# Kernel tuning notes

Measured on AMD Instinct MI355X. Metric: run time of the kernel, lower is better.

Reference implementation:

```python
import jax, jax.numpy as jnp
import numpy as np

N, E, F_IN, H, HEADS, L = 50000, 800000, 64, 64, 4, 5
NEG_SLOPE = 0.2  # PyG GATv2 default negative_slope


def _gatv2(h, src, dst, Wl, bl, Wr, br, att, bias, n):
    # PyG GATv2Conv, concat=False: x_l = lin_l(x), x_r = lin_r(x)
    xl = (h @ Wl + bl).reshape(n, HEADS, H)
    xr = (h @ Wr + br).reshape(n, HEADS, H)
    # per-edge score: a^T LeakyReLU(x_l[src] + x_r[dst])  -> [E', heads]
    z = jax.nn.leaky_relu(xl[src] + xr[dst], NEG_SLOPE)
    e = jnp.einsum('ehc,hc->eh', z, att)
    # segment softmax over incoming edges of each dst node
    m = jax.lax.stop_gradient(jax.ops.segment_max(e, dst, num_segments=n))
    ex = jnp.exp(e - m[dst])
    s = jax.ops.segment_sum(ex, dst, num_segments=n)
    alpha = ex / s[dst]
    out = jax.ops.segment_sum(xl[src] * alpha[:, :, None], dst, num_segments=n)
    return out.mean(axis=1) + bias  # concat=False -> mean over heads, + bias


def _forward(node_features, Wl, bl, Wr, br, att, gat_bias,
             Wm1, bm1, Wm2, bm2, Wp, bp, Wv1, bv1, Wv2, bv2,
             src, dst, current_pos, valid_neighbors, owned_nodes):
    n = node_features.shape[0]
    h = node_features
    for i in range(L):  # depth = 5 since N > 15
        h_new = jax.nn.elu(_gatv2(h, src, dst, Wl[i], bl[i], Wr[i], br[i], att[i], gat_bias[i], n))
        h = h_new if i == 0 else h + h_new  # residual after first layer
    cand = jnp.concatenate([jnp.asarray([current_pos], dtype=valid_neighbors.dtype), valid_neighbors])
    curr = h[current_pos]
    pairs = jnp.concatenate([jnp.broadcast_to(curr, (cand.shape[0], curr.shape[0])), h[cand]], axis=1)
    move_logits = (jax.nn.relu(pairs @ Wm1 + bm1) @ Wm2 + bm2)[:, 0]
    price_logits = h[owned_nodes] @ Wp + bp
    g = jnp.concatenate([h.mean(axis=0), curr])
    value = (jax.nn.relu(g @ Wv1 + bv1) @ Wv2 + bv2)[0]
    return move_logits, price_logits, value


def setup_inputs() -> dict:
    key = jax.random.key(0)
    ks = jax.random.split(key, 24)
    s = 0.05
    return {
        'node_features': jax.random.normal(ks[0], (N, F_IN), jnp.float32),
        'edge_index': jax.random.randint(ks[1], (2, E), 0, N),
        'current_pos': 7,
        'valid_neighbors': jax.random.randint(ks[2], (8,), 0, N),
        'owned_nodes': jax.random.randint(ks[3], (10,), 0, N),
        'Wl': jax.random.normal(ks[4], (L, F_IN, HEADS * H), jnp.float32) * s,
        'bl': jnp.zeros((L, HEADS * H), jnp.float32),
        'Wr': jax.random.normal(ks[5], (L, F_IN, HEADS * H), jnp.float32) * s,
        'br': jnp.zeros((L, HEADS * H), jnp.float32),
        'att': jax.random.normal(ks[6], (L, HEADS, H), jnp.float32) * s,
        'gat_bias': jnp.zeros((L, H), jnp.float32),
        'Wm1': jax.random.normal(ks[7], (2 * H, 128), jnp.float32) * s,
        'bm1': jnp.zeros((128,), jnp.float32),
        'Wm2': jax.random.normal(ks[8], (128, 1), jnp.float32) * s,
        'bm2': jnp.zeros((1,), jnp.float32),
        'Wp': jax.random.normal(ks[9], (H, 3), jnp.float32) * s,
        'bp': jnp.zeros((3,), jnp.float32),
        'Wv1': jax.random.normal(ks[10], (2 * H, 64), jnp.float32) * s,
        'bv1': jnp.zeros((64,), jnp.float32),
        'Wv2': jax.random.normal(ks[11], (64, 1), jnp.float32) * s,
        'bv2': jnp.zeros((1,), jnp.float32),
    }


def reference(node_features, edge_index, current_pos, valid_neighbors, owned_nodes,
              Wl, bl, Wr, br, att, gat_bias, Wm1, bm1, Wm2, bm2, Wp, bp, Wv1, bv1, Wv2, bv2):
    n = node_features.shape[0]
    loops = jnp.arange(n, dtype=edge_index.dtype)  # add_self_loops=True
    src = jnp.concatenate([edge_index[0], loops])
    dst = jnp.concatenate([edge_index[1], loops])
    return _forward(node_features, Wl, bl, Wr, br, att, gat_bias,
                    Wm1, bm1, Wm2, bm2, Wp, bp, Wv1, bv1, Wv2, bv2,
                    src, dst, current_pos, valid_neighbors, owned_nodes)
```

## Files before the change

### kernel.cpp

```cpp
#include <hip/hip_runtime.h>
#include <hip/hip_bf16.h>
#include <hip/hip_fp16.h>

#define NHID 256
#define HDIM 64
#define HEADS 4
#define LAYERS 5
#define LOG2E 1.4426950408889634f

using half8 = __attribute__((ext_vector_type(8))) _Float16;
using h2    = __attribute__((ext_vector_type(2))) _Float16;
using f32x4 = __attribute__((ext_vector_type(4))) float;

__global__ void count_deg(const int* __restrict__ dst, int* __restrict__ counts, int E, int n) {
    int i = blockIdx.x * blockDim.x + threadIdx.x;
    if (i < E) atomicAdd(&counts[dst[i]], 1);
    else if (i < E + n) atomicAdd(&counts[i - E], 1);
}

__global__ __launch_bounds__(256) void scan_partial(const int* __restrict__ counts,
                                                    int* __restrict__ out,
                                                    int* __restrict__ partials, int n) {
    __shared__ int buf[256];
    int tid = threadIdx.x;
    int i = blockIdx.x * 256 + tid;
    int v = (i < n) ? counts[i] : 0;
    buf[tid] = v;
    __syncthreads();
    for (int o = 1; o < 256; o <<= 1) {
        int t = (tid >= o) ? buf[tid - o] : 0;
        __syncthreads();
        buf[tid] += t;
        __syncthreads();
    }
    if (i < n) out[i] = buf[tid] - v;
    if (tid == 255) partials[blockIdx.x] = buf[255];
}

__global__ __launch_bounds__(256) void scan_partials_scan(int* __restrict__ partials,
                                                          int* __restrict__ out,
                                                          int nblk, int n) {
    __shared__ int buf[256];
    int tid = threadIdx.x;
    int v = (tid < nblk) ? partials[tid] : 0;
    buf[tid] = v;
    __syncthreads();
    for (int o = 1; o < 256; o <<= 1) {
        int t = (tid >= o) ? buf[tid - o] : 0;
        __syncthreads();
        buf[tid] += t;
        __syncthreads();
    }
    if (tid < nblk) partials[tid] = buf[tid] - v;
    if (tid == 255) out[n] = buf[255];
}

__global__ __launch_bounds__(256) void scan_add_offsets2(int* __restrict__ out,
                                                         int* __restrict__ out2,
                                                         const int* __restrict__ partials, int n) {
    int i = blockIdx.x * 256 + threadIdx.x;
    if (i < n) {
        int v = out[i] + partials[blockIdx.x];
        out[i] = v;
        out2[i] = v;
    }
}

__global__ void scatter_edges(const int* __restrict__ src, const int* __restrict__ dst,
                              int* __restrict__ row_fill, int* __restrict__ col_src, int E, int n) {
    int i = blockIdx.x * blockDim.x + threadIdx.x;
    if (i < E) {
        int p = atomicAdd(&row_fill[dst[i]], 1);
        col_src[p] = src[i] << 9;
    } else if (i < E + n) {
        int node = i - E;
        int p = atomicAdd(&row_fill[node], 1);
        col_src[p] = node << 9;
    }
}

__global__ __launch_bounds__(256) void wprep(const float* __restrict__ Wl,
                                             const float* __restrict__ Wr,
                                             __half* __restrict__ Wfrag) {
    int layer = blockIdx.x >> 4;
    int idx = (blockIdx.x & 15) * 256 + threadIdx.x;
    int t = idx >> 7, kh = (idx >> 6) & 1, lane = idx & 63;
    const float* WlL = Wl + (size_t)layer * 64 * 256;
    const float* WrL = Wr + (size_t)layer * 64 * 256;
    int col = t * 16 + (lane & 15);
    __half* outp = Wfrag + (size_t)layer * 32768 + ((size_t)(t * 2 + kh) * 64 + lane) * 8;
#pragma unroll
    for (int j = 0; j < 8; ++j) {
        int k = kh * 32 + (lane >> 4) * 8 + j;
        float v = (col < 256) ? WlL[k * 256 + col] : WrL[k * 256 + (col - 256)];
        outp[j] = __float2half(v);
    }
}

__global__ void conv_h16(const float* __restrict__ h, __half* __restrict__ h16, int total) {
    int i = blockIdx.x * blockDim.x + threadIdx.x;
    if (i < total) h16[i] = __float2half(h[i]);
}

__global__ __launch_bounds__(256) void gemm_mfma(const __half* __restrict__ h16,
                                                 const __half* __restrict__ Wfrag,
                                                 const float* __restrict__ bl,
                                                 const float* __restrict__ br,
                                                 __half* __restrict__ xlh,
                                                 __half* __restrict__ xrh, int n) {
    int w = threadIdx.x >> 6, l = threadIdx.x & 63;
    int row0 = blockIdx.x * 64 + w * 16;
    if (row0 >= n) return;
    int arow = row0 + (l & 15);
    half8 A0 = *(const half8*)(h16 + (size_t)arow * 64 + (l >> 4) * 8);
    half8 A1 = *(const half8*)(h16 + (size_t)arow * 64 + 32 + (l >> 4) * 8);
    int orow = row0 + (l >> 4) * 4;
#pragma unroll
    for (int t = 0; t < 32; ++t) {
        half8 B0 = *(const half8*)(Wfrag + ((size_t)(t * 2 + 0) * 64 + l) * 8);
        half8 B1 = *(const half8*)(Wfrag + ((size_t)(t * 2 + 1) * 64 + l) * 8);
        f32x4 acc = {0.f, 0.f, 0.f, 0.f};
        acc = __builtin_amdgcn_mfma_f32_16x16x32_f16(A0, B0, acc, 0, 0, 0);
        acc = __builtin_amdgcn_mfma_f32_16x16x32_f16(A1, B1, acc, 0, 0, 0);
        int col = t * 16 + (l & 15);
        if (col < 256) {
            float b = bl[col];
#pragma unroll
            for (int j = 0; j < 4; ++j)
                xlh[(size_t)(orow + j) * 256 + col] = __float2half(acc[j] + b);
        } else {
            float b = br[col - 256];
#pragma unroll
            for (int j = 0; j < 4; ++j)
                xrh[(size_t)(orow + j) * 256 + (col - 256)] = __float2half(acc[j] + b);
        }
    }
}

template <int CTRL>
__device__ __forceinline__ float dpp_mov_f32(float x) {
    return __int_as_float(__builtin_amdgcn_update_dpp(0, __float_as_int(x), CTRL, 0xf, 0xf, false));
}
__device__ __forceinline__ float group16_reduce_add(float x) {
    x += dpp_mov_f32<0xB1>(x);
    x += dpp_mov_f32<0x4E>(x);
    x += dpp_mov_f32<0x124>(x);
    x += dpp_mov_f32<0x128>(x);
    return x;
}

__global__ __launch_bounds__(256) void gat_node(const __half* __restrict__ xlh,
                                                const __half* __restrict__ xrh,
                                                const int* __restrict__ row_ptr,
                                                const int* __restrict__ col_src,
                                                const float* __restrict__ att,
                                                const float* __restrict__ gbias,
                                                const float* __restrict__ h_res,
                                                float* __restrict__ h_out,
                                                __half* __restrict__ h16_out, int n) {
    int wid  = threadIdx.x >> 6;
    int lane = threadIdx.x & 63;
    int node = blockIdx.x * 4 + wid;
    if (node >= n) return;

    const char* xlb = (const char*)xlh;
    int laneoff = lane << 3;

    uint2 xrp = ((const uint2*)(xrh + (size_t)node * NHID))[lane];
    h2 xr01 = __builtin_bit_cast(h2, xrp.x);
    h2 xr23 = __builtin_bit_cast(h2, xrp.y);

    float4 av = ((const float4*)att)[lane];
    av.x *= LOG2E; av.y *= LOG2E; av.z *= LOG2E; av.w *= LOG2E;
    h2 c02 = {(_Float16)0.2f, (_Float16)0.2f};

    float m = -INFINITY, s = 0.f;
    float4 acc = make_float4(0.f, 0.f, 0.f, 0.f);

    int e0 = row_ptr[node], e1 = row_ptr[node + 1];
    uint2 x0 = *(const uint2*)(xlb + (size_t)(unsigned)col_src[e0 + 0] + laneoff);
    uint2 x1 = *(const uint2*)(xlb + (size_t)(unsigned)col_src[e0 + 1] + laneoff);
    uint2 x2 = *(const uint2*)(xlb + (size_t)(unsigned)col_src[e0 + 2] + laneoff);
    uint2 x3 = *(const uint2*)(xlb + (size_t)(unsigned)col_src[e0 + 3] + laneoff);

    for (int idx = e0; idx < e1; ++idx) {
        uint2 raw = x0;
        x0 = x1; x1 = x2; x2 = x3;
        x3 = *(const uint2*)(xlb + (size_t)(unsigned)col_src[idx + 4] + laneoff);

        h2 cur01 = __builtin_bit_cast(h2, raw.x);
        h2 cur23 = __builtin_bit_cast(h2, raw.y);
        h2 z01 = cur01 + xr01;
        h2 z23 = cur23 + xr23;
        z01 = __builtin_elementwise_max(z01, z01 * c02);
        z23 = __builtin_elementwise_max(z23, z23 * c02);

        float pp;
        pp = (float)z01.x * av.x;
        pp = fmaf((float)z01.y, av.y, pp);
        pp = fmaf((float)z23.x, av.z, pp);
        pp = fmaf((float)z23.y, av.w, pp);
        pp = group16_reduce_add(pp);

        if (__any(pp > m + 11.541560f)) {
            float mn = fmaxf(m, pp);
            float f  = exp2f(m - mn);
            float w  = exp2f(pp - mn);
            acc.x = fmaf((float)cur01.x, w, acc.x * f);
            acc.y = fmaf((float)cur01.y, w, acc.y * f);
            acc.z = fmaf((float)cur23.x, w, acc.z * f);
            acc.w = fmaf((float)cur23.y, w, acc.w * f);
            s = s * f + w;
            m = mn;
        } else {
            float w = exp2f(pp - m);
            acc.x = fmaf((float)cur01.x, w, acc.x);
            acc.y = fmaf((float)cur01.y, w, acc.y);
            acc.z = fmaf((float)cur23.x, w, acc.z);
            acc.w = fmaf((float)cur23.y, w, acc.w);
            s += w;
        }
    }

    float inv = 1.0f / s;
    float4 v = make_float4(acc.x * inv, acc.y * inv, acc.z * inv, acc.w * inv);
    v.x += __shfl_xor(v.x, 16, 64); v.y += __shfl_xor(v.y, 16, 64);
    v.z += __shfl_xor(v.z, 16, 64); v.w += __shfl_xor(v.w, 16, 64);
    v.x += __shfl_xor(v.x, 32, 64); v.y += __shfl_xor(v.y, 32, 64);
    v.z += __shfl_xor(v.z, 32, 64); v.w += __shfl_xor(v.w, 32, 64);

    if (lane < 16) {
        float4 g = ((const float4*)gbias)[lane];
        float4 o;
        o.x = v.x * 0.25f + g.x;
        o.y = v.y * 0.25f + g.y;
        o.z = v.z * 0.25f + g.z;
        o.w = v.w * 0.25f + g.w;
        o.x = (o.x > 0.f) ? o.x : expm1f(o.x);
        o.y = (o.y > 0.f) ? o.y : expm1f(o.y);
        o.z = (o.z > 0.f) ? o.z : expm1f(o.z);
        o.w = (o.w > 0.f) ? o.w : expm1f(o.w);
        if (h_res) {
            float4 r = ((const float4*)(h_res + (size_t)node * 64))[lane];
            o.x += r.x; o.y += r.y; o.z += r.z; o.w += r.w;
        }
        ((float4*)(h_out + (size_t)node * 64))[lane] = o;
        __half2 p0 = __float22half2_rn(make_float2(o.x, o.y));
        __half2 p1 = __float22half2_rn(make_float2(o.z, o.w));
        uint2 pk;
        pk.x = *(unsigned*)&p0;
        pk.y = *(unsigned*)&p1;
        ((uint2*)(h16_out + (size_t)node * 64))[lane] = pk;
    }
}

__global__ __launch_bounds__(256) void col_sum(const float* __restrict__ h,
                                               float* __restrict__ gsum, int n) {
    int col = threadIdx.x & 63;
    int sub = threadIdx.x >> 6;
    float s = 0.f;
    for (int r = blockIdx.x * 4 + sub; r < n; r += gridDim.x * 4)
        s += h[(size_t)r * 64 + col];
    __shared__ float tmp[4][64];
    tmp[sub][col] = s;
    __syncthreads();
    if (threadIdx.x < 64) {
        int t = threadIdx.x;
        atomicAdd(&gsum[t], tmp[0][t] + tmp[1][t] + tmp[2][t] + tmp[3][t]);
    }
}

__global__ __launch_bounds__(128) void heads_kernel(const float* __restrict__ h,
                                                    const float* __restrict__ gsum,
                                                    const int* __restrict__ cur_pos,
                                                    const int* __restrict__ valid,
                                                    const int* __restrict__ owned,
                                                    const float* __restrict__ Wm1, const float* __restrict__ bm1,
                                                    const float* __restrict__ Wm2, const float* __restrict__ bm2,
                                                    const float* __restrict__ Wp,  const float* __restrict__ bp,
                                                    const float* __restrict__ Wv1, const float* __restrict__ bv1,
                                                    const float* __restrict__ Wv2, const float* __restrict__ bv2,
                                                    float* __restrict__ out, int n) {
    int blk = blockIdx.x;
    int tid = threadIdx.x;
    int pos = cur_pos[0];

    if (blk < 9) {
        int cand = (blk == 0) ? pos : valid[blk - 1];
        const float* hcur  = h + (size_t)pos  * 64;
        const float* hcand = h + (size_t)cand * 64;
        float a = bm1[tid];
#pragma unroll
        for (int k = 0; k < 64; ++k) a += hcur[k]  * Wm1[k * 128 + tid];
#pragma unroll
        for (int k = 0; k < 64; ++k) a += hcand[k] * Wm1[(64 + k) * 128 + tid];
        a = fmaxf(a, 0.f) * Wm2[tid];
#pragma unroll
        for (int o = 1; o < 64; o <<= 1) a += __shfl_xor(a, o, 64);
        __shared__ float red[2];
        if ((tid & 63) == 0) red[tid >> 6] = a;
        __syncthreads();
        if (tid == 0) out[blk] = red[0] + red[1] + bm2[0];
    } else if (blk == 9) {
        if (tid < 30) {
            int i = tid / 3, cc = tid % 3;
            int node = owned[i];
            const float* hn = h + (size_t)node * 64;
            float a = bp[cc];
#pragma unroll
            for (int k = 0; k < 64; ++k) a += hn[k] * Wp[k * 3 + cc];
            out[9 + tid] = a;
        }
    } else {
        float invn = 1.0f / (float)n;
        const float* hcur = h + (size_t)pos * 64;
        float a = 0.f;
        if (tid < 64) {
            a = bv1[tid];
#pragma unroll
            for (int k = 0; k < 64; ++k) a += (gsum[k] * invn) * Wv1[k * 64 + tid];
#pragma unroll
            for (int k = 0; k < 64; ++k) a += hcur[k] * Wv1[(64 + k) * 64 + tid];
            a = fmaxf(a, 0.f) * Wv2[tid];
#pragma unroll
            for (int o = 1; o < 64; o <<= 1) a += __shfl_xor(a, o, 64);
            if (tid == 0) out[39] = a + bv2[0];
        }
    }
}

extern "C" void kernel_launch(void* const* d_in, const int* in_sizes, int n_in,
                              void* d_out, int out_size, void* d_ws, size_t ws_size,
                              hipStream_t stream) {
    const float* nf    = (const float*)d_in[0];
    const int*   ei    = (const int*)d_in[1];
    const int*   cpos  = (const int*)d_in[2];
    const int*   valid = (const int*)d_in[3];
    const int*   owned = (const int*)d_in[4];
    const float* Wl    = (const float*)d_in[5];
    const float* bl    = (const float*)d_in[6];
    const float* Wr    = (const float*)d_in[7];
    const float* br    = (const float*)d_in[8];
    const float* att   = (const float*)d_in[9];
    const float* gbias = (const float*)d_in[10];
    const float* Wm1 = (const float*)d_in[11];
    const float* bm1 = (const float*)d_in[12];
    const float* Wm2 = (const float*)d_in[13];
    const float* bm2 = (const float*)d_in[14];
    const float* Wp  = (const float*)d_in[15];
    const float* bp  = (const float*)d_in[16];
    const float* Wv1 = (const float*)d_in[17];
    const float* bv1 = (const float*)d_in[18];
    const float* Wv2 = (const float*)d_in[19];
    const float* bv2 = (const float*)d_in[20];
    float* out = (float*)d_out;

    int n = in_sizes[0] / 64;
    int E = in_sizes[1] / 2;
    const int* srcp = ei;
    const int* dstp = ei + E;

    char* w = (char*)d_ws;
    auto alloc = [&](size_t bytes) -> char* {
        char* p = w;
        w += (bytes + 255) & ~(size_t)255;
        return p;
    };
    __half* xlh     = (__half*)alloc((size_t)n * NHID * 2);
    __half* xrh     = (__half*)alloc((size_t)n * NHID * 2);
    float* hA       = (float*)alloc((size_t)n * 64 * 4);
    float* hB       = (float*)alloc((size_t)n * 64 * 4);
    __half* h16     = (__half*)alloc((size_t)n * 64 * 2);
    __half* Wfrag   = (__half*)alloc((size_t)LAYERS * 32768 * 2);
    float* gsum     = (float*)alloc(64 * 4);
    int*   row_ptr  = (int*)alloc((size_t)(n + 1) * 4);
    int*   row_fill = (int*)alloc((size_t)n * 4);
    int*   col_src  = (int*)alloc((size_t)(E + n + 16) * 4);
    int*   partials = (int*)alloc(256 * 4);

    int nblk = (n + 255) / 256;
    int nthr = E + n;

    hipMemsetAsync(row_fill, 0, (size_t)n * 4, stream);
    count_deg<<<(nthr + 255) / 256, 256, 0, stream>>>(dstp, row_fill, E, n);
    scan_partial<<<nblk, 256, 0, stream>>>(row_fill, row_ptr, partials, n);
    scan_partials_scan<<<1, 256, 0, stream>>>(partials, row_ptr, nblk, n);
    scan_add_offsets2<<<nblk, 256, 0, stream>>>(row_ptr, row_fill, partials, n);
    scatter_edges<<<(nthr + 255) / 256, 256, 0, stream>>>(srcp, dstp, row_fill, col_src, E, n);
    hipMemsetAsync(col_src + E + n, 0, 16 * 4, stream);

    wprep<<<LAYERS * 16, 256, 0, stream>>>(Wl, Wr, Wfrag);
    conv_h16<<<(n * 64 + 255) / 256, 256, 0, stream>>>(nf, h16, n * 64);

    const float* hin = nf;
    float* hnext = hB;
    for (int i = 0; i < LAYERS; ++i) {
        gemm_mfma<<<(n + 63) / 64, 256, 0, stream>>>(h16, Wfrag + (size_t)i * 32768,
                                                     bl + i * 256, br + i * 256,
                                                     xlh, xrh, n);
        const float* res = (i == 0) ? nullptr : hin;
        float* outp = (i == 0) ? hA : hnext;
        gat_node<<<(n + 3) / 4, 256, 0, stream>>>(xlh, xrh, row_ptr, col_src,
                                                  att + i * HEADS * 64, gbias + i * 64,
                                                  res, outp, h16, n);
        if (i == 0) {
            hin = hA; hnext = hB;
        } else {
            const float* t = hin;
            hin = outp;
            hnext = (float*)t;
        }
    }

    hipMemsetAsync(gsum, 0, 64 * 4, stream);
    col_sum<<<256, 256, 0, stream>>>(hin, gsum, n);
    heads_kernel<<<11, 128, 0, stream>>>(hin, gsum, cpos, valid, owned,
                                         Wm1, bm1, Wm2, bm2, Wp, bp,
                                         Wv1, bv1, Wv2, bv2, out, n);
}
```

Baseline: 761.9 us.

## Process two edges per wavefront iteration with half-waves and 16-byte gathers

The GAT aggregation kernel now splits each 64-lane wavefront into two half-waves. Each half handles a different incoming edge, with every lane gathering 16 bytes (8 halfs) instead of 8. The two halves keep separate online-softmax states and merge them at the end through cross-half shuffles with max rescaling. This halves the loop trip count and widens each gather, at the cost of more registers, extra shuffles in the epilogue, and masking for odd degree counts.

```diff
diff --git a/kernel.cpp b/kernel.cpp
--- a/kernel.cpp
+++ b/kernel.cpp
@@ -141,13 +141,6 @@
 __device__ __forceinline__ float dpp_mov_f32(float x) {
     return __int_as_float(__builtin_amdgcn_update_dpp(0, __float_as_int(x), CTRL, 0xf, 0xf, false));
 }
-__device__ __forceinline__ float group16_reduce_add(float x) {
-    x += dpp_mov_f32<0xB1>(x);
-    x += dpp_mov_f32<0x4E>(x);
-    x += dpp_mov_f32<0x124>(x);
-    x += dpp_mov_f32<0x128>(x);
-    return x;
-}
 
 __global__ __launch_bounds__(256) void gat_node(const __half* __restrict__ xlh,
                                                 const __half* __restrict__ xrh,
@@ -159,98 +152,146 @@
                                                 float* __restrict__ h_out,
                                                 __half* __restrict__ h16_out, int n) {
     int wid  = threadIdx.x >> 6;
-    int lane = threadIdx.x & 63;
+    int l    = threadIdx.x & 63;
     int node = blockIdx.x * 4 + wid;
     if (node >= n) return;
+    int ll   = l & 31;
+    bool hi  = l >= 32;
+    int laneoff = ll << 4;
 
     const char* xlb = (const char*)xlh;
-    int laneoff = lane << 3;
-
-    uint2 xrp = ((const uint2*)(xrh + (size_t)node * NHID))[lane];
-    h2 xr01 = __builtin_bit_cast(h2, xrp.x);
-    h2 xr23 = __builtin_bit_cast(h2, xrp.y);
-
-    float4 av = ((const float4*)att)[lane];
-    av.x *= LOG2E; av.y *= LOG2E; av.z *= LOG2E; av.w *= LOG2E;
+    uint4 xrp = *(const uint4*)((const char*)xrh + (size_t)node * 512 + laneoff);
+    h2 xr0 = __builtin_bit_cast(h2, xrp.x);
+    h2 xr1 = __builtin_bit_cast(h2, xrp.y);
+    h2 xr2 = __builtin_bit_cast(h2, xrp.z);
+    h2 xr3 = __builtin_bit_cast(h2, xrp.w);
+
+    const float* ap = att + (ll >> 3) * 64 + (ll & 7) * 8;
+    float4 avA = *(const float4*)ap;
+    float4 avB = *(const float4*)(ap + 4);
+    avA.x *= LOG2E; avA.y *= LOG2E; avA.z *= LOG2E; avA.w *= LOG2E;
+    avB.x *= LOG2E; avB.y *= LOG2E; avB.z *= LOG2E; avB.w *= LOG2E;
+
     h2 c02 = {(_Float16)0.2f, (_Float16)0.2f};
-
-    float m = -INFINITY, s = 0.f;
-    float4 acc = make_float4(0.f, 0.f, 0.f, 0.f);
+    const float NEGBIG = -1.0e30f;
+    float m = NEGBIG, s = 0.f;
+    float a0=0.f,a1=0.f,a2=0.f,a3=0.f,a4=0.f,a5=0.f,a6=0.f,a7=0.f;
 
     int e0 = row_ptr[node], e1 = row_ptr[node + 1];
-    uint2 x0 = *(const uint2*)(xlb + (size_t)(unsigned)col_src[e0 + 0] + laneoff);
-    uint2 x1 = *(const uint2*)(xlb + (size_t)(unsigned)col_src[e0 + 1] + laneoff);
-    uint2 x2 = *(const uint2*)(xlb + (size_t)(unsigned)col_src[e0 + 2] + laneoff);
-    uint2 x3 = *(const uint2*)(xlb + (size_t)(unsigned)col_src[e0 + 3] + laneoff);
-
-    for (int idx = e0; idx < e1; ++idx) {
-        uint2 raw = x0;
-        x0 = x1; x1 = x2; x2 = x3;
-        x3 = *(const uint2*)(xlb + (size_t)(unsigned)col_src[idx + 4] + laneoff);
-
-        h2 cur01 = __builtin_bit_cast(h2, raw.x);
-        h2 cur23 = __builtin_bit_cast(h2, raw.y);
-        h2 z01 = cur01 + xr01;
-        h2 z23 = cur23 + xr23;
-        z01 = __builtin_elementwise_max(z01, z01 * c02);
-        z23 = __builtin_elementwise_max(z23, z23 * c02);
+    int2 cA = *(const int2*)(col_src + e0);
+    uint4 xa = *(const uint4*)(xlb + (size_t)(unsigned)(hi ? cA.y : cA.x) + laneoff);
+    int2 cB = *(const int2*)(col_src + e0 + 2);
+    uint4 xb = *(const uint4*)(xlb + (size_t)(unsigned)(hi ? cB.y : cB.x) + laneoff);
+
+    for (int idx = e0; idx < e1; idx += 2) {
+        uint4 raw = xa;
+        xa = xb;
+        int2 cz = *(const int2*)(col_src + idx + 4);
+        xb = *(const uint4*)(xlb + (size_t)(unsigned)(hi ? cz.y : cz.x) + laneoff);
+
+        h2 u0 = __builtin_bit_cast(h2, raw.x);
+        h2 u1 = __builtin_bit_cast(h2, raw.y);
+        h2 u2 = __builtin_bit_cast(h2, raw.z);
+        h2 u3 = __builtin_bit_cast(h2, raw.w);
+        h2 z0 = u0 + xr0, z1 = u1 + xr1, z2 = u2 + xr2, z3 = u3 + xr3;
+        z0 = __builtin_elementwise_max(z0, z0 * c02);
+        z1 = __builtin_elementwise_max(z1, z1 * c02);
+        z2 = __builtin_elementwise_max(z2, z2 * c02);
+        z3 = __builtin_elementwise_max(z3, z3 * c02);
 
         float pp;
-        pp = (float)z01.x * av.x;
-        pp = fmaf((float)z01.y, av.y, pp);
-        pp = fmaf((float)z23.x, av.z, pp);
-        pp = fmaf((float)z23.y, av.w, pp);
-        pp = group16_reduce_add(pp);
+        pp =  (float)z0.x * avA.x;
+        pp = fmaf((float)z0.y, avA.y, pp);
+        pp = fmaf((float)z1.x, avA.z, pp);
+        pp = fmaf((float)z1.y, avA.w, pp);
+        pp = fmaf((float)z2.x, avB.x, pp);
+        pp = fmaf((float)z2.y, avB.y, pp);
+        pp = fmaf((float)z3.x, avB.z, pp);
+        pp = fmaf((float)z3.y, avB.w, pp);
+        pp += dpp_mov_f32<0xB1>(pp);
+        pp += dpp_mov_f32<0x4E>(pp);
+        pp += __shfl_xor(pp, 4, 64);
+        if (hi && (idx + 1 >= e1)) pp = NEGBIG;
 
         if (__any(pp > m + 11.541560f)) {
             float mn = fmaxf(m, pp);
             float f  = exp2f(m - mn);
             float w  = exp2f(pp - mn);
-            acc.x = fmaf((float)cur01.x, w, acc.x * f);
-            acc.y = fmaf((float)cur01.y, w, acc.y * f);
-            acc.z = fmaf((float)cur23.x, w, acc.z * f);
-            acc.w = fmaf((float)cur23.y, w, acc.w * f);
+            a0 = fmaf((float)u0.x, w, a0 * f); a1 = fmaf((float)u0.y, w, a1 * f);
+            a2 = fmaf((float)u1.x, w, a2 * f); a3 = fmaf((float)u1.y, w, a3 * f);
+            a4 = fmaf((float)u2.x, w, a4 * f); a5 = fmaf((float)u2.y, w, a5 * f);
+            a6 = fmaf((float)u3.x, w, a6 * f); a7 = fmaf((float)u3.y, w, a7 * f);
             s = s * f + w;
             m = mn;
         } else {
             float w = exp2f(pp - m);
-            acc.x = fmaf((float)cur01.x, w, acc.x);
-            acc.y = fmaf((float)cur01.y, w, acc.y);
-            acc.z = fmaf((float)cur23.x, w, acc.z);
-            acc.w = fmaf((float)cur23.y, w, acc.w);
+            a0 = fmaf((float)u0.x, w, a0); a1 = fmaf((float)u0.y, w, a1);
+            a2 = fmaf((float)u1.x, w, a2); a3 = fmaf((float)u1.y, w, a3);
+            a4 = fmaf((float)u2.x, w, a4); a5 = fmaf((float)u2.y, w, a5);
+            a6 = fmaf((float)u3.x, w, a6); a7 = fmaf((float)u3.y, w, a7);
             s += w;
         }
     }
 
-    float inv = 1.0f / s;
-    float4 v = make_float4(acc.x * inv, acc.y * inv, acc.z * inv, acc.w * inv);
-    v.x += __shfl_xor(v.x, 16, 64); v.y += __shfl_xor(v.y, 16, 64);
-    v.z += __shfl_xor(v.z, 16, 64); v.w += __shfl_xor(v.w, 16, 64);
-    v.x += __shfl_xor(v.x, 32, 64); v.y += __shfl_xor(v.y, 32, 64);
-    v.z += __shfl_xor(v.z, 32, 64); v.w += __shfl_xor(v.w, 32, 64);
-
-    if (lane < 16) {
-        float4 g = ((const float4*)gbias)[lane];
-        float4 o;
-        o.x = v.x * 0.25f + g.x;
-        o.y = v.y * 0.25f + g.y;
-        o.z = v.z * 0.25f + g.z;
-        o.w = v.w * 0.25f + g.w;
-        o.x = (o.x > 0.f) ? o.x : expm1f(o.x);
-        o.y = (o.y > 0.f) ? o.y : expm1f(o.y);
-        o.z = (o.z > 0.f) ? o.z : expm1f(o.z);
-        o.w = (o.w > 0.f) ? o.w : expm1f(o.w);
+    float m2 = __shfl_xor(m, 32, 64);
+    float s2 = __shfl_xor(s, 32, 64);
+    float M  = fmaxf(m, m2);
+    float f0 = exp2f(m - M), f1 = exp2f(m2 - M);
+    float v0 = a0 * f0 + __shfl_xor(a0, 32, 64) * f1;
+    float v1 = a1 * f0 + __shfl_xor(a1, 32, 64) * f1;
+    float v2 = a2 * f0 + __shfl_xor(a2, 32, 64) * f1;
+    float v3 = a3 * f0 + __shfl_xor(a3, 32, 64) * f1;
+    float v4 = a4 * f0 + __shfl_xor(a4, 32, 64) * f1;
+    float v5 = a5 * f0 + __shfl_xor(a5, 32, 64) * f1;
+    float v6 = a6 * f0 + __shfl_xor(a6, 32, 64) * f1;
+    float v7 = a7 * f0 + __shfl_xor(a7, 32, 64) * f1;
+    float sT = s * f0 + s2 * f1;
+    float inv = 1.0f / sT;
+    v0 *= inv; v1 *= inv; v2 *= inv; v3 *= inv;
+    v4 *= inv; v5 *= inv; v6 *= inv; v7 *= inv;
+    v0 += __shfl_xor(v0, 8, 64); v1 += __shfl_xor(v1, 8, 64);
+    v2 += __shfl_xor(v2, 8, 64); v3 += __shfl_xor(v3, 8, 64);
+    v4 += __shfl_xor(v4, 8, 64); v5 += __shfl_xor(v5, 8, 64);
+    v6 += __shfl_xor(v6, 8, 64); v7 += __shfl_xor(v7, 8, 64);
+    v0 += __shfl_xor(v0, 16, 64); v1 += __shfl_xor(v1, 16, 64);
+    v2 += __shfl_xor(v2, 16, 64); v3 += __shfl_xor(v3, 16, 64);
+    v4 += __shfl_xor(v4, 16, 64); v5 += __shfl_xor(v5, 16, 64);
+    v6 += __shfl_xor(v6, 16, 64); v7 += __shfl_xor(v7, 16, 64);
+
+    if (l < 8) {
+        const float* gp = gbias + l * 8;
+        float4 gA = *(const float4*)gp;
+        float4 gB = *(const float4*)(gp + 4);
+        float o0 = v0 * 0.25f + gA.x, o1 = v1 * 0.25f + gA.y;
+        float o2 = v2 * 0.25f + gA.z, o3 = v3 * 0.25f + gA.w;
+        float o4 = v4 * 0.25f + gB.x, o5 = v5 * 0.25f + gB.y;
+        float o6 = v6 * 0.25f + gB.z, o7 = v7 * 0.25f + gB.w;
+        o0 = (o0 > 0.f) ? o0 : exp2f(o0 * LOG2E) - 1.f;
+        o1 = (o1 > 0.f) ? o1 : exp2f(o1 * LOG2E) - 1.f;
+        o2 = (o2 > 0.f) ? o2 : exp2f(o2 * LOG2E) - 1.f;
+        o3 = (o3 > 0.f) ? o3 : exp2f(o3 * LOG2E) - 1.f;
+        o4 = (o4 > 0.f) ? o4 : exp2f(o4 * LOG2E) - 1.f;
+        o5 = (o5 > 0.f) ? o5 : exp2f(o5 * LOG2E) - 1.f;
+        o6 = (o6 > 0.f) ? o6 : exp2f(o6 * LOG2E) - 1.f;
+        o7 = (o7 > 0.f) ? o7 : exp2f(o7 * LOG2E) - 1.f;
         if (h_res) {
-            float4 r = ((const float4*)(h_res + (size_t)node * 64))[lane];
-            o.x += r.x; o.y += r.y; o.z += r.z; o.w += r.w;
-        }
-        ((float4*)(h_out + (size_t)node * 64))[lane] = o;
-        __half2 p0 = __float22half2_rn(make_float2(o.x, o.y));
-        __half2 p1 = __float22half2_rn(make_float2(o.z, o.w));
-        uint2 pk;
-        pk.x = *(unsigned*)&p0;
-        pk.y = *(unsigned*)&p1;
-        ((uint2*)(h16_out + (size_t)node * 64))[lane] = pk;
+            const float* rp = h_res + (size_t)node * 64 + l * 8;
+            float4 rA = *(const float4*)rp;
+            float4 rB = *(const float4*)(rp + 4);
+            o0 += rA.x; o1 += rA.y; o2 += rA.z; o3 += rA.w;
+            o4 += rB.x; o5 += rB.y; o6 += rB.z; o7 += rB.w;
+        }
+        float* op = h_out + (size_t)node * 64 + l * 8;
+        *(float4*)op       = make_float4(o0, o1, o2, o3);
+        *(float4*)(op + 4) = make_float4(o4, o5, o6, o7);
+        __half2 p0 = __float22half2_rn(make_float2(o0, o1));
+        __half2 p1 = __float22half2_rn(make_float2(o2, o3));
+        __half2 p2 = __float22half2_rn(make_float2(o4, o5));
+        __half2 p3 = __float22half2_rn(make_float2(o6, o7));
+        uint4 pk;
+        pk.x = *(unsigned*)&p0; pk.y = *(unsigned*)&p1;
+        pk.z = *(unsigned*)&p2; pk.w = *(unsigned*)&p3;
+        *(uint4*)((char*)h16_out + (size_t)node * 128 + l * 16) = pk;
     }
 }
 
```

After: 660.2 us. -13.4%, faster.

## Process four edges per wavefront iteration with per-lane 16-channel slices

Applied to the files above, without the earlier changes.

The GAT aggregation kernel is restructured so each wavefront handles four edges at once, one per 16-lane group, and each lane owns 16 channels instead of 4. Each group keeps its own online-softmax state, and the groups are merged with cross-lane shuffles at the end, followed by a reduction over heads. The aim is fewer loop iterations, wider 32-byte gathers and less DPP reduction per edge. In exchange it uses more registers (16 accumulators plus fp16 attention weights), adds a merge epilogue, and relies on col_src padding for reads past the edge range.

```diff
diff --git a/kernel.cpp b/kernel.cpp
--- a/kernel.cpp
+++ b/kernel.cpp
@@ -11,6 +11,8 @@
 using half8 = __attribute__((ext_vector_type(8))) _Float16;
 using h2    = __attribute__((ext_vector_type(2))) _Float16;
 using f32x4 = __attribute__((ext_vector_type(4))) float;
+
+#define BC(x) __builtin_bit_cast(h2, x)
 
 __global__ void count_deg(const int* __restrict__ dst, int* __restrict__ counts, int E, int n) {
     int i = blockIdx.x * blockDim.x + threadIdx.x;
@@ -141,13 +143,6 @@
 __device__ __forceinline__ float dpp_mov_f32(float x) {
     return __int_as_float(__builtin_amdgcn_update_dpp(0, __float_as_int(x), CTRL, 0xf, 0xf, false));
 }
-__device__ __forceinline__ float group16_reduce_add(float x) {
-    x += dpp_mov_f32<0xB1>(x);
-    x += dpp_mov_f32<0x4E>(x);
-    x += dpp_mov_f32<0x124>(x);
-    x += dpp_mov_f32<0x128>(x);
-    return x;
-}
 
 __global__ __launch_bounds__(256) void gat_node(const __half* __restrict__ xlh,
                                                 const __half* __restrict__ xrh,
@@ -159,98 +154,149 @@
                                                 float* __restrict__ h_out,
                                                 __half* __restrict__ h16_out, int n) {
     int wid  = threadIdx.x >> 6;
-    int lane = threadIdx.x & 63;
+    int l    = threadIdx.x & 63;
     int node = blockIdx.x * 4 + wid;
     if (node >= n) return;
+    int j = l & 15;
+    int e = l >> 4;
+    int laneoff = j << 5;
 
     const char* xlb = (const char*)xlh;
-    int laneoff = lane << 3;
-
-    uint2 xrp = ((const uint2*)(xrh + (size_t)node * NHID))[lane];
-    h2 xr01 = __builtin_bit_cast(h2, xrp.x);
-    h2 xr23 = __builtin_bit_cast(h2, xrp.y);
-
-    float4 av = ((const float4*)att)[lane];
-    av.x *= LOG2E; av.y *= LOG2E; av.z *= LOG2E; av.w *= LOG2E;
+    const char* xrb = (const char*)xrh + (size_t)node * 512 + laneoff;
+    uint4 xq0 = *(const uint4*)xrb;
+    uint4 xq1 = *(const uint4*)(xrb + 16);
+    h2 xr[8];
+    xr[0] = BC(xq0.x); xr[1] = BC(xq0.y); xr[2] = BC(xq0.z); xr[3] = BC(xq0.w);
+    xr[4] = BC(xq1.x); xr[5] = BC(xq1.y); xr[6] = BC(xq1.z); xr[7] = BC(xq1.w);
+
+    const float* ap = att + j * 16;
+    h2 av[8];
+#pragma unroll
+    for (int k = 0; k < 8; ++k) {
+        av[k].x = (_Float16)(ap[2 * k]     * LOG2E);
+        av[k].y = (_Float16)(ap[2 * k + 1] * LOG2E);
+    }
+
     h2 c02 = {(_Float16)0.2f, (_Float16)0.2f};
-
-    float m = -INFINITY, s = 0.f;
-    float4 acc = make_float4(0.f, 0.f, 0.f, 0.f);
+    const float NEGBIG = -1.0e30f;
+    float m = NEGBIG, s = 0.f;
+    float ac[16];
+#pragma unroll
+    for (int k = 0; k < 16; ++k) ac[k] = 0.f;
 
     int e0 = row_ptr[node], e1 = row_ptr[node + 1];
-    uint2 x0 = *(const uint2*)(xlb + (size_t)(unsigned)col_src[e0 + 0] + laneoff);
-    uint2 x1 = *(const uint2*)(xlb + (size_t)(unsigned)col_src[e0 + 1] + laneoff);
-    uint2 x2 = *(const uint2*)(xlb + (size_t)(unsigned)col_src[e0 + 2] + laneoff);
-    uint2 x3 = *(const uint2*)(xlb + (size_t)(unsigned)col_src[e0 + 3] + laneoff);
-
-    for (int idx = e0; idx < e1; ++idx) {
-        uint2 raw = x0;
-        x0 = x1; x1 = x2; x2 = x3;
-        x3 = *(const uint2*)(xlb + (size_t)(unsigned)col_src[idx + 4] + laneoff);
-
-        h2 cur01 = __builtin_bit_cast(h2, raw.x);
-        h2 cur23 = __builtin_bit_cast(h2, raw.y);
-        h2 z01 = cur01 + xr01;
-        h2 z23 = cur23 + xr23;
-        z01 = __builtin_elementwise_max(z01, z01 * c02);
-        z23 = __builtin_elementwise_max(z23, z23 * c02);
-
-        float pp;
-        pp = (float)z01.x * av.x;
-        pp = fmaf((float)z01.y, av.y, pp);
-        pp = fmaf((float)z23.x, av.z, pp);
-        pp = fmaf((float)z23.y, av.w, pp);
-        pp = group16_reduce_add(pp);
+    int off0 = col_src[e0 + e];
+    uint4 xa0 = *(const uint4*)(xlb + (size_t)(unsigned)off0 + laneoff);
+    uint4 xa1 = *(const uint4*)(xlb + (size_t)(unsigned)off0 + laneoff + 16);
+    int off1 = col_src[e0 + 4 + e];
+    uint4 xb0 = *(const uint4*)(xlb + (size_t)(unsigned)off1 + laneoff);
+    uint4 xb1 = *(const uint4*)(xlb + (size_t)(unsigned)off1 + laneoff + 16);
+
+    for (int base = e0; base < e1; base += 4) {
+        uint4 r0 = xa0, r1 = xa1;
+        xa0 = xb0; xa1 = xb1;
+        int off2 = col_src[base + 8 + e];
+        xb0 = *(const uint4*)(xlb + (size_t)(unsigned)off2 + laneoff);
+        xb1 = *(const uint4*)(xlb + (size_t)(unsigned)off2 + laneoff + 16);
+
+        h2 u[8];
+        u[0] = BC(r0.x); u[1] = BC(r0.y); u[2] = BC(r0.z); u[3] = BC(r0.w);
+        u[4] = BC(r1.x); u[5] = BC(r1.y); u[6] = BC(r1.z); u[7] = BC(r1.w);
+
+        float pp = 0.f;
+#pragma unroll
+        for (int k = 0; k < 8; ++k) {
+            h2 z = u[k] + xr[k];
+            z = __builtin_elementwise_max(z, z * c02);
+            pp = fmaf((float)z.x, (float)av[k].x, pp);
+            pp = fmaf((float)z.y, (float)av[k].y, pp);
+        }
+        pp += dpp_mov_f32<0xB1>(pp);
+        pp += dpp_mov_f32<0x4E>(pp);
+        if (base + e >= e1) pp = NEGBIG;
 
         if (__any(pp > m + 11.541560f)) {
             float mn = fmaxf(m, pp);
             float f  = exp2f(m - mn);
             float w  = exp2f(pp - mn);
-            acc.x = fmaf((float)cur01.x, w, acc.x * f);
-            acc.y = fmaf((float)cur01.y, w, acc.y * f);
-            acc.z = fmaf((float)cur23.x, w, acc.z * f);
-            acc.w = fmaf((float)cur23.y, w, acc.w * f);
+#pragma unroll
+            for (int k = 0; k < 8; ++k) {
+                ac[2 * k]     = fmaf((float)u[k].x, w, ac[2 * k] * f);
+                ac[2 * k + 1] = fmaf((float)u[k].y, w, ac[2 * k + 1] * f);
+            }
             s = s * f + w;
             m = mn;
         } else {
             float w = exp2f(pp - m);
-            acc.x = fmaf((float)cur01.x, w, acc.x);
-            acc.y = fmaf((float)cur01.y, w, acc.y);
-            acc.z = fmaf((float)cur23.x, w, acc.z);
-            acc.w = fmaf((float)cur23.y, w, acc.w);
+#pragma unroll
+            for (int k = 0; k < 8; ++k) {
+                ac[2 * k]     = fmaf((float)u[k].x, w, ac[2 * k]);
+                ac[2 * k + 1] = fmaf((float)u[k].y, w, ac[2 * k + 1]);
+            }
             s += w;
         }
     }
 
+    {
+        float m2 = __shfl_xor(m, 16, 64);
+        float s2 = __shfl_xor(s, 16, 64);
+        float M  = fmaxf(m, m2);
+        float f0 = exp2f(m - M), f1 = exp2f(m2 - M);
+#pragma unroll
+        for (int k = 0; k < 16; ++k)
+            ac[k] = ac[k] * f0 + __shfl_xor(ac[k], 16, 64) * f1;
+        s = s * f0 + s2 * f1;
+        m = M;
+    }
+    {
+        float m2 = __shfl_xor(m, 32, 64);
+        float s2 = __shfl_xor(s, 32, 64);
+        float M  = fmaxf(m, m2);
+        float f0 = exp2f(m - M), f1 = exp2f(m2 - M);
+#pragma unroll
+        for (int k = 0; k < 16; ++k)
+            ac[k] = ac[k] * f0 + __shfl_xor(ac[k], 32, 64) * f1;
+        s = s * f0 + s2 * f1;
+        m = M;
+    }
     float inv = 1.0f / s;
-    float4 v = make_float4(acc.x * inv, acc.y * inv, acc.z * inv, acc.w * inv);
-    v.x += __shfl_xor(v.x, 16, 64); v.y += __shfl_xor(v.y, 16, 64);
-    v.z += __shfl_xor(v.z, 16, 64); v.w += __shfl_xor(v.w, 16, 64);
-    v.x += __shfl_xor(v.x, 32, 64); v.y += __shfl_xor(v.y, 32, 64);
-    v.z += __shfl_xor(v.z, 32, 64); v.w += __shfl_xor(v.w, 32, 64);
-
-    if (lane < 16) {
-        float4 g = ((const float4*)gbias)[lane];
-        float4 o;
-        o.x = v.x * 0.25f + g.x;
-        o.y = v.y * 0.25f + g.y;
-        o.z = v.z * 0.25f + g.z;
-        o.w = v.w * 0.25f + g.w;
-        o.x = (o.x > 0.f) ? o.x : expm1f(o.x);
-        o.y = (o.y > 0.f) ? o.y : expm1f(o.y);
-        o.z = (o.z > 0.f) ? o.z : expm1f(o.z);
-        o.w = (o.w > 0.f) ? o.w : expm1f(o.w);
+#pragma unroll
+    for (int k = 0; k < 16; ++k) ac[k] *= inv;
+#pragma unroll
+    for (int k = 0; k < 16; ++k) ac[k] += __shfl_xor(ac[k], 4, 64);
+#pragma unroll
+    for (int k = 0; k < 16; ++k) ac[k] += __shfl_xor(ac[k], 8, 64);
+
+    if (l < 4) {
+        const float* gp = gbias + l * 16;
+        float o[16];
+#pragma unroll
+        for (int k = 0; k < 16; ++k) {
+            float t = ac[k] * 0.25f + gp[k];
+            o[k] = (t > 0.f) ? t : exp2f(t * LOG2E) - 1.f;
+        }
         if (h_res) {
-            float4 r = ((const float4*)(h_res + (size_t)node * 64))[lane];
-            o.x += r.x; o.y += r.y; o.z += r.z; o.w += r.w;
-        }
-        ((float4*)(h_out + (size_t)node * 64))[lane] = o;
-        __half2 p0 = __float22half2_rn(make_float2(o.x, o.y));
-        __half2 p1 = __float22half2_rn(make_float2(o.z, o.w));
-        uint2 pk;
-        pk.x = *(unsigned*)&p0;
-        pk.y = *(unsigned*)&p1;
-        ((uint2*)(h16_out + (size_t)node * 64))[lane] = pk;
+            const float* rp = h_res + (size_t)node * 64 + l * 16;
+#pragma unroll
+            for (int k = 0; k < 16; ++k) o[k] += rp[k];
+        }
+        float* op = h_out + (size_t)node * 64 + l * 16;
+#pragma unroll
+        for (int k = 0; k < 4; ++k)
+            *(float4*)(op + 4 * k) = make_float4(o[4 * k], o[4 * k + 1], o[4 * k + 2], o[4 * k + 3]);
+        uint4 pk0, pk1;
+        __half2 t0, t1;
+        t0 = __float22half2_rn(make_float2(o[0], o[1]));  pk0.x = *(unsigned*)&t0;
+        t1 = __float22half2_rn(make_float2(o[2], o[3]));  pk0.y = *(unsigned*)&t1;
+        t0 = __float22half2_rn(make_float2(o[4], o[5]));  pk0.z = *(unsigned*)&t0;
+        t1 = __float22half2_rn(make_float2(o[6], o[7]));  pk0.w = *(unsigned*)&t1;
+        t0 = __float22half2_rn(make_float2(o[8], o[9]));  pk1.x = *(unsigned*)&t0;
+        t1 = __float22half2_rn(make_float2(o[10], o[11])); pk1.y = *(unsigned*)&t1;
+        t0 = __float22half2_rn(make_float2(o[12], o[13])); pk1.z = *(unsigned*)&t0;
+        t1 = __float22half2_rn(make_float2(o[14], o[15])); pk1.w = *(unsigned*)&t1;
+        char* hp = (char*)h16_out + (size_t)node * 128 + l * 32;
+        *(uint4*)hp        = pk0;
+        *(uint4*)(hp + 16) = pk1;
     }
 }
 
```

Result: faster. 744.8 us (-2.2%).
